# Kernel optimization log

Hardware: AMD Instinct MI355X
Metric: run time of the kernel (lower is better)

The kernel has to match this reference:

```python
import jax, jax.numpy as jnp
import numpy as np

C = 3               # BSARec cutoff hyperparameter
CUTOFF = max(1, C // 2 + 1)  # number of low-frequency bins kept = 2
LN_EPS = 1e-5       # torch LayerNorm default


def setup_inputs() -> dict:
    key = jax.random.key(0)
    k1, k2 = jax.random.split(key)
    B, S, H = 64, 2048, 256
    x = jax.random.normal(k1, (B, S, H), dtype=jnp.float32)
    sqrt_beta = jax.random.normal(k2, (1, 1, H), dtype=jnp.float32)
    ln_weight = jnp.ones((H,), dtype=jnp.float32)
    ln_bias = jnp.zeros((H,), dtype=jnp.float32)
    return {"x": x, "sqrt_beta": sqrt_beta, "ln_weight": ln_weight, "ln_bias": ln_bias}


def _layer_norm(h, weight, bias):
    mean = jnp.mean(h, axis=-1, keepdims=True)
    var = jnp.mean(jnp.square(h - mean), axis=-1, keepdims=True)
    return (h - mean) * jax.lax.rsqrt(var + LN_EPS) * weight + bias


def reference(x, sqrt_beta, ln_weight, ln_bias):
    B, S, H = x.shape
    # orthonormal rFFT along the sequence axis
    x_fft = jnp.fft.rfft(x, axis=1, norm="ortho")          # [B, S//2+1, H] complex
    freq_bins = x_fft.shape[1]
    cutoff = min(freq_bins, CUTOFF)
    # zero all bins >= cutoff (low-pass)
    bin_idx = jnp.arange(freq_bins)[None, :, None]
    low_fft = jnp.where(bin_idx < cutoff, x_fft, 0.0 + 0.0j)
    low_pass = jnp.fft.irfft(low_fft, n=S, axis=1, norm="ortho")  # [B, S, H]
    high_pass = x - low_pass
    seq = low_pass + jnp.square(sqrt_beta) * high_pass
    # dropout is identity at eval time
    return _layer_norm(seq + x, ln_weight, ln_bias)
```

## Files before the change

### kernel.cpp

```cpp
#include <hip/hip_runtime.h>

#define B_DIM 64
#define S_LEN 2048
#define H_DIM 256
#define TWO_PI 6.283185307179586f

typedef float f32x4 __attribute__((ext_vector_type(4)));

__global__ __launch_bounds__(256) void k_partial(const float* __restrict__ x,
                                                 float* __restrict__ partials,
                                                 int rows_per_split) {
    const int b = blockIdx.x;
    const int split = blockIdx.y;
    const int tid = threadIdx.x;
    const int lane = tid & 63;
    const int wave = tid >> 6;
    const int h0 = lane * 4;

    float s0[4] = {0.f, 0.f, 0.f, 0.f};
    float c1[4] = {0.f, 0.f, 0.f, 0.f};
    float s1[4] = {0.f, 0.f, 0.f, 0.f};

    const int t_begin = split * rows_per_split;
    const int t_end = t_begin + rows_per_split;
    const float wfreq = TWO_PI / (float)S_LEN;

    for (int t = t_begin + wave; t < t_end; t += 4) {
        const f32x4 v = *reinterpret_cast<const f32x4*>(
            x + ((size_t)b * S_LEN + t) * H_DIM + h0);
        float sn, cs;
        __sincosf(wfreq * (float)t, &sn, &cs);
        s0[0] += v.x;      s0[1] += v.y;      s0[2] += v.z;      s0[3] += v.w;
        c1[0] += v.x * cs; c1[1] += v.y * cs; c1[2] += v.z * cs; c1[3] += v.w * cs;
        s1[0] += v.x * sn; s1[1] += v.y * sn; s1[2] += v.z * sn; s1[3] += v.w * sn;
    }

    __shared__ float red[4][3 * H_DIM];
#pragma unroll
    for (int j = 0; j < 4; ++j) {
        red[wave][0 * H_DIM + h0 + j] = s0[j];
        red[wave][1 * H_DIM + h0 + j] = c1[j];
        red[wave][2 * H_DIM + h0 + j] = s1[j];
    }
    __syncthreads();

#pragma unroll
    for (int k = 0; k < 3; ++k) {
        const int v = tid + k * 256;
        const float acc = red[0][v] + red[1][v] + red[2][v] + red[3][v];
        __builtin_nontemporal_store(
            acc, &partials[((size_t)(split * B_DIM + b)) * (3 * H_DIM) + v]);
    }
}

__global__ __launch_bounds__(256) void k_reduce(const float* __restrict__ partials,
                                                float* __restrict__ sums,
                                                int nsplit) {
    const int j = blockIdx.x * 256 + threadIdx.x;
    float acc = 0.f;
    for (int s = 0; s < nsplit; ++s)
        acc += partials[(size_t)s * (B_DIM * 3 * H_DIM) + j];
    sums[j] = acc;
}

#define ROWS_PER_BLOCK 16
__global__ __launch_bounds__(256) void k_final(const float* __restrict__ x,
                                               const float* __restrict__ sums,
                                               const float* __restrict__ sqrt_beta,
                                               const float* __restrict__ lnw,
                                               const float* __restrict__ lnb,
                                               float* __restrict__ out) {
    const int blocks_per_b = S_LEN / ROWS_PER_BLOCK;
    const int b = blockIdx.x / blocks_per_b;
    const int tchunk = blockIdx.x % blocks_per_b;
    const int tid = threadIdx.x;
    const int lane = tid & 63;
    const int wave = tid >> 6;

    __shared__ float sS0[H_DIM], sC1[H_DIM], sS1[H_DIM];
    __shared__ float sCA[H_DIM], sCB[H_DIM], sW[H_DIM], sBi[H_DIM];
    {
        const int h = tid;
        sS0[h] = sums[b * 768 + h];
        sC1[h] = sums[b * 768 + 256 + h];
        sS1[h] = sums[b * 768 + 512 + h];
        const float sb = sqrt_beta[h];
        const float b2 = sb * sb;
        sCA[h] = 1.f + b2;
        sCB[h] = 1.f - b2;
        sW[h] = lnw[h];
        sBi[h] = lnb[h];
    }
    __syncthreads();

    const float invS = 1.f / (float)S_LEN;
    const float wfreq = TWO_PI / (float)S_LEN;
    const int h0 = lane * 4;

#pragma unroll
    for (int r = 0; r < ROWS_PER_BLOCK / 4; ++r) {
        const int t = tchunk * ROWS_PER_BLOCK + wave * (ROWS_PER_BLOCK / 4) + r;
        float sn, cs;
        __sincosf(wfreq * (float)t, &sn, &cs);

        const size_t base = ((size_t)b * S_LEN + t) * H_DIM + h0;
        const f32x4 v = *reinterpret_cast<const f32x4*>(x + base);
        const float xf[4] = {v.x, v.y, v.z, v.w};

        float y[4];
        float sum = 0.f, sumsq = 0.f;
#pragma unroll
        for (int j = 0; j < 4; ++j) {
            const int h = h0 + j;
            const float lp = invS * (sS0[h] + 2.f * (sC1[h] * cs + sS1[h] * sn));
            const float yy = sCB[h] * lp + sCA[h] * xf[j];
            y[j] = yy;
            sum += yy;
            sumsq += yy * yy;
        }
#pragma unroll
        for (int m = 1; m < 64; m <<= 1) {
            sum += __shfl_xor(sum, m, 64);
            sumsq += __shfl_xor(sumsq, m, 64);
        }
        const float mean = sum * (1.f / (float)H_DIM);
        const float var = sumsq * (1.f / (float)H_DIM) - mean * mean;
        const float rstd = rsqrtf(var + 1e-5f);

        f32x4 o;
        o.x = (y[0] - mean) * rstd * sW[h0 + 0] + sBi[h0 + 0];
        o.y = (y[1] - mean) * rstd * sW[h0 + 1] + sBi[h0 + 1];
        o.z = (y[2] - mean) * rstd * sW[h0 + 2] + sBi[h0 + 2];
        o.w = (y[3] - mean) * rstd * sW[h0 + 3] + sBi[h0 + 3];
        __builtin_nontemporal_store(o, reinterpret_cast<f32x4*>(out + base));
    }
}

extern "C" void kernel_launch(void* const* d_in, const int* in_sizes, int n_in,
                              void* d_out, int out_size, void* d_ws, size_t ws_size,
                              hipStream_t stream) {
    const float* x  = (const float*)d_in[0];
    const float* sb = (const float*)d_in[1];
    const float* w  = (const float*)d_in[2];
    const float* bi = (const float*)d_in[3];
    float* out = (float*)d_out;

    int nsplit = 16;
    while (nsplit > 1 &&
           ((size_t)(nsplit + 1) * B_DIM * 3 * H_DIM * sizeof(float)) > ws_size)
        nsplit >>= 1;
    float* partials = (float*)d_ws;
    float* sums = partials + (size_t)nsplit * B_DIM * 3 * H_DIM;

    k_partial<<<dim3(B_DIM, nsplit), 256, 0, stream>>>(x, partials, S_LEN / nsplit);
    k_reduce<<<(B_DIM * 3 * H_DIM) / 256, 256, 0, stream>>>(partials, sums, nsplit);
    k_final<<<B_DIM * (S_LEN / ROWS_PER_BLOCK), 256, 0, stream>>>(x, sums, sb, w, bi, out);
}
```

Baseline: 74.46 us.

## Fuse partial, reduce and final kernels into one cooperative kernel with grid sync

Replaces the three-kernel pipeline (partial Fourier sums, split reduction, LayerNorm output) with a single cooperative kernel of 1024 blocks of 512 threads. Each block computes its slice's DC and first-harmonic sums, writes them to workspace, grid-syncs, then re-reduces the 16 partials for its batch and processes the same 128 rows. The same block re-reads the rows it summed, so the second read may hit in cache, and two launches are removed. The cost is a grid-wide barrier and the need for all blocks to be co-resident, with the old path kept as a fallback if the cooperative launch fails.

```diff
diff --git a/kernel.cpp b/kernel.cpp
--- a/kernel.cpp
+++ b/kernel.cpp
@@ -1,11 +1,134 @@
 #include <hip/hip_runtime.h>
+#include <hip/hip_cooperative_groups.h>
+
+namespace cg = cooperative_groups;
 
 #define B_DIM 64
 #define S_LEN 2048
 #define H_DIM 256
 #define TWO_PI 6.283185307179586f
 
+#define NBLK 1024
+#define NTHR 512
+#define NWAVE 8
+#define ROWS_PER_BLK 128
+
 typedef float f32x4 __attribute__((ext_vector_type(4)));
+
+__global__ __launch_bounds__(NTHR, 8) void k_fused(const float* __restrict__ x,
+                                                   const float* __restrict__ sqrt_beta,
+                                                   const float* __restrict__ lnw,
+                                                   const float* __restrict__ lnb,
+                                                   float* __restrict__ out,
+                                                   float* __restrict__ ws) {
+    const int blk = blockIdx.x;
+    const int b = blk >> 4;
+    const int q = blk & 15;
+    const int tid = threadIdx.x;
+    const int lane = tid & 63;
+    const int wave = tid >> 6;
+    const int h0 = lane * 4;
+
+    const float wfreq = TWO_PI / (float)S_LEN;
+    const int t_base = q * ROWS_PER_BLK;
+    const float* __restrict__ px = x + ((size_t)b * S_LEN + t_base) * H_DIM + h0;
+
+    __shared__ float red[NWAVE][3 * H_DIM];
+
+    f32x4 s0v = {0.f, 0.f, 0.f, 0.f};
+    f32x4 c1v = {0.f, 0.f, 0.f, 0.f};
+    f32x4 s1v = {0.f, 0.f, 0.f, 0.f};
+#pragma unroll
+    for (int kk = 0; kk < ROWS_PER_BLK / 32; ++kk) {
+        const int r0 = wave + kk * 32;
+        const f32x4 v0 = *reinterpret_cast<const f32x4*>(px + (size_t)(r0     ) * H_DIM);
+        const f32x4 v1 = *reinterpret_cast<const f32x4*>(px + (size_t)(r0 +  8) * H_DIM);
+        const f32x4 v2 = *reinterpret_cast<const f32x4*>(px + (size_t)(r0 + 16) * H_DIM);
+        const f32x4 v3 = *reinterpret_cast<const f32x4*>(px + (size_t)(r0 + 24) * H_DIM);
+        float sn0, cs0, sn1, cs1, sn2, cs2, sn3, cs3;
+        __sincosf(wfreq * (float)(t_base + r0     ), &sn0, &cs0);
+        __sincosf(wfreq * (float)(t_base + r0 +  8), &sn1, &cs1);
+        __sincosf(wfreq * (float)(t_base + r0 + 16), &sn2, &cs2);
+        __sincosf(wfreq * (float)(t_base + r0 + 24), &sn3, &cs3);
+        s0v += (v0 + v1) + (v2 + v3);
+        c1v += (v0 * cs0 + v1 * cs1) + (v2 * cs2 + v3 * cs3);
+        s1v += (v0 * sn0 + v1 * sn1) + (v2 * sn2 + v3 * sn3);
+    }
+
+#pragma unroll
+    for (int j = 0; j < 4; ++j) {
+        red[wave][0 * H_DIM + h0 + j] = s0v[j];
+        red[wave][1 * H_DIM + h0 + j] = c1v[j];
+        red[wave][2 * H_DIM + h0 + j] = s1v[j];
+    }
+    __syncthreads();
+    for (int j = tid; j < 3 * H_DIM; j += NTHR) {
+        float acc = 0.f;
+#pragma unroll
+        for (int w = 0; w < NWAVE; ++w) acc += red[w][j];
+        ws[(size_t)blk * (3 * H_DIM) + j] = acc;
+    }
+
+    cg::this_grid().sync();
+
+    const int pbase = blk & ~15;
+    for (int j = tid; j < 3 * H_DIM; j += NTHR) {
+        float acc = 0.f;
+#pragma unroll
+        for (int k = 0; k < 16; ++k)
+            acc += ws[(size_t)(pbase + k) * (3 * H_DIM) + j];
+        red[0][j] = acc;
+    }
+    __syncthreads();
+
+    const f32x4 S0 = *reinterpret_cast<const f32x4*>(&red[0][h0]);
+    const f32x4 C1 = *reinterpret_cast<const f32x4*>(&red[0][H_DIM + h0]);
+    const f32x4 S1 = *reinterpret_cast<const f32x4*>(&red[0][2 * H_DIM + h0]);
+    const f32x4 sb = *reinterpret_cast<const f32x4*>(sqrt_beta + h0);
+    const f32x4 Wv = *reinterpret_cast<const f32x4*>(lnw + h0);
+    const f32x4 Bv = *reinterpret_cast<const f32x4*>(lnb + h0);
+    const f32x4 b2 = sb * sb;
+    const f32x4 CA = b2 + 1.f;
+    const f32x4 CB = 1.f - b2;
+    const float invS = 1.f / (float)S_LEN;
+
+    float* __restrict__ po = out + ((size_t)b * S_LEN + t_base) * H_DIM + h0;
+#pragma unroll
+    for (int k = 0; k < ROWS_PER_BLK / NWAVE; k += 2) {
+        const int r0 = wave + k * NWAVE;
+        const int r1 = wave + (k + 1) * NWAVE;
+        const f32x4 va = *reinterpret_cast<const f32x4*>(px + (size_t)r0 * H_DIM);
+        const f32x4 vb = *reinterpret_cast<const f32x4*>(px + (size_t)r1 * H_DIM);
+        float sna, csa, snb, csb;
+        __sincosf(wfreq * (float)(t_base + r0), &sna, &csa);
+        __sincosf(wfreq * (float)(t_base + r1), &snb, &csb);
+        const f32x4 ya = CB * ((S0 + (C1 * csa + S1 * sna) * 2.f) * invS) + CA * va;
+        const f32x4 yb = CB * ((S0 + (C1 * csb + S1 * snb) * 2.f) * invS) + CA * vb;
+
+        float suma = ya.x + ya.y + ya.z + ya.w;
+        float sqa  = ya.x * ya.x + ya.y * ya.y + ya.z * ya.z + ya.w * ya.w;
+        float sumb = yb.x + yb.y + yb.z + yb.w;
+        float sqb  = yb.x * yb.x + yb.y * yb.y + yb.z * yb.z + yb.w * yb.w;
+#pragma unroll
+        for (int m = 1; m < 64; m <<= 1) {
+            suma += __shfl_xor(suma, m, 64);
+            sqa  += __shfl_xor(sqa,  m, 64);
+            sumb += __shfl_xor(sumb, m, 64);
+            sqb  += __shfl_xor(sqb,  m, 64);
+        }
+        const float meana = suma * (1.f / (float)H_DIM);
+        const float vara = sqa * (1.f / (float)H_DIM) - meana * meana;
+        const float rstda = rsqrtf(vara + 1e-5f);
+        const float meanb = sumb * (1.f / (float)H_DIM);
+        const float varb = sqb * (1.f / (float)H_DIM) - meanb * meanb;
+        const float rstdb = rsqrtf(varb + 1e-5f);
+
+        f32x4 oa = (ya - meana) * rstda * Wv + Bv;
+        f32x4 ob = (yb - meanb) * rstdb * Wv + Bv;
+        __builtin_nontemporal_store(oa, reinterpret_cast<f32x4*>(po + (size_t)r0 * H_DIM));
+        __builtin_nontemporal_store(ob, reinterpret_cast<f32x4*>(po + (size_t)r1 * H_DIM));
+    }
+}
 
 __global__ __launch_bounds__(256) void k_partial(const float* __restrict__ x,
                                                  float* __restrict__ partials,
@@ -17,9 +140,9 @@
     const int wave = tid >> 6;
     const int h0 = lane * 4;
 
-    float s0[4] = {0.f, 0.f, 0.f, 0.f};
-    float c1[4] = {0.f, 0.f, 0.f, 0.f};
-    float s1[4] = {0.f, 0.f, 0.f, 0.f};
+    f32x4 s0v = {0.f, 0.f, 0.f, 0.f};
+    f32x4 c1v = {0.f, 0.f, 0.f, 0.f};
+    f32x4 s1v = {0.f, 0.f, 0.f, 0.f};
 
     const int t_begin = split * rows_per_split;
     const int t_end = t_begin + rows_per_split;
@@ -30,26 +153,24 @@
             x + ((size_t)b * S_LEN + t) * H_DIM + h0);
         float sn, cs;
         __sincosf(wfreq * (float)t, &sn, &cs);
-        s0[0] += v.x;      s0[1] += v.y;      s0[2] += v.z;      s0[3] += v.w;
-        c1[0] += v.x * cs; c1[1] += v.y * cs; c1[2] += v.z * cs; c1[3] += v.w * cs;
-        s1[0] += v.x * sn; s1[1] += v.y * sn; s1[2] += v.z * sn; s1[3] += v.w * sn;
+        s0v += v;
+        c1v += v * cs;
+        s1v += v * sn;
     }
 
     __shared__ float red[4][3 * H_DIM];
 #pragma unroll
     for (int j = 0; j < 4; ++j) {
-        red[wave][0 * H_DIM + h0 + j] = s0[j];
-        red[wave][1 * H_DIM + h0 + j] = c1[j];
-        red[wave][2 * H_DIM + h0 + j] = s1[j];
-    }
-    __syncthreads();
-
+        red[wave][0 * H_DIM + h0 + j] = s0v[j];
+        red[wave][1 * H_DIM + h0 + j] = c1v[j];
+        red[wave][2 * H_DIM + h0 + j] = s1v[j];
+    }
+    __syncthreads();
 #pragma unroll
     for (int k = 0; k < 3; ++k) {
         const int v = tid + k * 256;
-        const float acc = red[0][v] + red[1][v] + red[2][v] + red[3][v];
-        __builtin_nontemporal_store(
-            acc, &partials[((size_t)(split * B_DIM + b)) * (3 * H_DIM) + v]);
+        partials[((size_t)(split * B_DIM + b)) * (3 * H_DIM) + v] =
+            red[0][v] + red[1][v] + red[2][v] + red[3][v];
     }
 }
 
@@ -63,14 +184,14 @@
     sums[j] = acc;
 }
 
-#define ROWS_PER_BLOCK 16
+#define FB_ROWS 16
 __global__ __launch_bounds__(256) void k_final(const float* __restrict__ x,
                                                const float* __restrict__ sums,
                                                const float* __restrict__ sqrt_beta,
                                                const float* __restrict__ lnw,
                                                const float* __restrict__ lnb,
                                                float* __restrict__ out) {
-    const int blocks_per_b = S_LEN / ROWS_PER_BLOCK;
+    const int blocks_per_b = S_LEN / FB_ROWS;
     const int b = blockIdx.x / blocks_per_b;
     const int tchunk = blockIdx.x % blocks_per_b;
     const int tid = threadIdx.x;
@@ -84,8 +205,8 @@
         sS0[h] = sums[b * 768 + h];
         sC1[h] = sums[b * 768 + 256 + h];
         sS1[h] = sums[b * 768 + 512 + h];
-        const float sb = sqrt_beta[h];
-        const float b2 = sb * sb;
+        const float s = sqrt_beta[h];
+        const float b2 = s * s;
         sCA[h] = 1.f + b2;
         sCB[h] = 1.f - b2;
         sW[h] = lnw[h];
@@ -98,14 +219,13 @@
     const int h0 = lane * 4;
 
 #pragma unroll
-    for (int r = 0; r < ROWS_PER_BLOCK / 4; ++r) {
-        const int t = tchunk * ROWS_PER_BLOCK + wave * (ROWS_PER_BLOCK / 4) + r;
+    for (int r = 0; r < FB_ROWS / 4; ++r) {
+        const int t = tchunk * FB_ROWS + wave * (FB_ROWS / 4) + r;
         float sn, cs;
         __sincosf(wfreq * (float)t, &sn, &cs);
 
         const size_t base = ((size_t)b * S_LEN + t) * H_DIM + h0;
         const f32x4 v = *reinterpret_cast<const f32x4*>(x + base);
-        const float xf[4] = {v.x, v.y, v.z, v.w};
 
         float y[4];
         float sum = 0.f, sumsq = 0.f;
@@ -113,7 +233,7 @@
         for (int j = 0; j < 4; ++j) {
             const int h = h0 + j;
             const float lp = invS * (sS0[h] + 2.f * (sC1[h] * cs + sS1[h] * sn));
-            const float yy = sCB[h] * lp + sCA[h] * xf[j];
+            const float yy = sCB[h] * lp + sCA[h] * v[j];
             y[j] = yy;
             sum += yy;
             sumsq += yy * yy;
@@ -132,7 +252,7 @@
         o.y = (y[1] - mean) * rstd * sW[h0 + 1] + sBi[h0 + 1];
         o.z = (y[2] - mean) * rstd * sW[h0 + 2] + sBi[h0 + 2];
         o.w = (y[3] - mean) * rstd * sW[h0 + 3] + sBi[h0 + 3];
-        __builtin_nontemporal_store(o, reinterpret_cast<f32x4*>(out + base));
+        *reinterpret_cast<f32x4*>(out + base) = o;
     }
 }
 
@@ -144,15 +264,21 @@
     const float* w  = (const float*)d_in[2];
     const float* bi = (const float*)d_in[3];
     float* out = (float*)d_out;
-
-    int nsplit = 16;
-    while (nsplit > 1 &&
-           ((size_t)(nsplit + 1) * B_DIM * 3 * H_DIM * sizeof(float)) > ws_size)
-        nsplit >>= 1;
-    float* partials = (float*)d_ws;
-    float* sums = partials + (size_t)nsplit * B_DIM * 3 * H_DIM;
-
-    k_partial<<<dim3(B_DIM, nsplit), 256, 0, stream>>>(x, partials, S_LEN / nsplit);
-    k_reduce<<<(B_DIM * 3 * H_DIM) / 256, 256, 0, stream>>>(partials, sums, nsplit);
-    k_final<<<B_DIM * (S_LEN / ROWS_PER_BLOCK), 256, 0, stream>>>(x, sums, sb, w, bi, out);
-}
+    float* ws = (float*)d_ws;
+
+    void* args[] = {(void*)&x, (void*)&sb, (void*)&w, (void*)&bi,
+                    (void*)&out, (void*)&ws};
+    hipError_t err = hipLaunchCooperativeKernel((const void*)k_fused, dim3(NBLK),
+                                                dim3(NTHR), args, 0, stream);
+    if (err != hipSuccess) {
+        int nsplit = 16;
+        while (nsplit > 1 &&
+               ((size_t)(nsplit + 1) * B_DIM * 3 * H_DIM * sizeof(float)) > ws_size)
+            nsplit >>= 1;
+        float* partials = (float*)d_ws;
+        float* sums = partials + (size_t)nsplit * B_DIM * 3 * H_DIM;
+        k_partial<<<dim3(B_DIM, nsplit), 256, 0, stream>>>(x, partials, S_LEN / nsplit);
+        k_reduce<<<(B_DIM * 3 * H_DIM) / 256, 256, 0, stream>>>(partials, sums, nsplit);
+        k_final<<<B_DIM * (S_LEN / FB_ROWS), 256, 0, stream>>>(x, sums, sb, w, bi, out);
+    }
+}
```

Result: slower. 217.7 us (+192.4%).
